# Performance work log

Hardware: AMD Instinct MI355X
Metric: run time of the kernel (lower is better)

## Reference

```python
import jax, jax.numpy as jnp
import numpy as np

EMBED = 1024
HEADS = 16
HEAD_DIM = EMBED // HEADS


def setup_inputs() -> dict:
    key = jax.random.key(0)
    ks = jax.random.split(key, 8)
    N, S = 4, 2048
    inp = {
        "values": jax.random.normal(ks[0], (N, S, EMBED), jnp.float32),
        "keys": jax.random.normal(ks[1], (N, S, EMBED), jnp.float32),
        "queries": jax.random.normal(ks[2], (N, S, EMBED), jnp.float32),
        "mask": jnp.ones((N, S), jnp.int32),  # unused by the original forward
        # learned params (torch Linear: y = x @ W.T + b)
        "Wv": jax.random.normal(ks[3], (HEAD_DIM, HEAD_DIM), jnp.float32) / np.sqrt(HEAD_DIM),
        "Wk": jax.random.normal(ks[4], (HEAD_DIM, HEAD_DIM), jnp.float32) / np.sqrt(HEAD_DIM),
        "Wq": jax.random.normal(ks[5], (HEAD_DIM, HEAD_DIM), jnp.float32) / np.sqrt(HEAD_DIM),
        "Wo": jax.random.normal(ks[6], (EMBED, EMBED), jnp.float32) / np.sqrt(EMBED),
        "bo": jax.random.normal(ks[7], (EMBED,), jnp.float32) * 0.01,
    }
    return inp


def reference(values, keys, queries, mask, Wv, Wk, Wq, Wo, bo):
    N, S, _ = queries.shape
    # reshape to (N, len, heads, head_dim)
    v = values.reshape(N, S, HEADS, HEAD_DIM)
    k = keys.reshape(N, S, HEADS, HEAD_DIM)
    q = queries.reshape(N, S, HEADS, HEAD_DIM)
    # per-head linear projections (weights shared across heads), y = x @ W.T
    v = jnp.einsum('nlhd,ed->nlhe', v, Wv)
    k = jnp.einsum('nlhd,ed->nlhe', k, Wk)
    q = jnp.einsum('nlhd,ed->nlhe', q, Wq)
    # attention scores scaled by sqrt(embed_size), faithful to original
    scores = jnp.einsum('nqhd,nkhd->nhqk', q, k) / jnp.sqrt(jnp.float32(EMBED))
    attn = jax.nn.softmax(scores, axis=3)
    out = jnp.einsum('nhql,nlhd->nqhd', attn, v).reshape(N, S, EMBED)
    return out @ Wo.T + bo
```

## Files before the change

### kernel.cpp

```cpp
#include <hip/hip_runtime.h>


using f32x4  = __attribute__((ext_vector_type(4))) float;
using f32x16 = __attribute__((ext_vector_type(16))) float;
using bf16x8 = __attribute__((ext_vector_type(8))) __bf16;
using u32x4  = __attribute__((ext_vector_type(4))) unsigned int;
using u16x8  = __attribute__((ext_vector_type(8))) unsigned short;
typedef unsigned short u16;
typedef unsigned int   u32;
typedef unsigned long long u64;

#define SEQ 2048
#define EMB 1024
#define NHEADS 16
#define HDIM 64
#define NBATCH 4
#define NH 64

__device__ __forceinline__ u16 f2bf(float f) {
  u32 u = __builtin_bit_cast(u32, f);
  return (u16)((u + 0x7fffu + ((u >> 16) & 1u)) >> 16);
}

__device__ __forceinline__ u32 cvtpk_bf16(float a, float b) {
  u32 d;
  asm("v_cvt_pk_bf16_f32 %0, %1, %2" : "=v"(d) : "v"(a), "v"(b));
  return d;
}

__device__ __forceinline__ f32x4 mfma16(bf16x8 a, bf16x8 b, f32x4 c) {
  return __builtin_amdgcn_mfma_f32_16x16x32_bf16(a, b, c, 0, 0, 0);
}

__device__ __forceinline__ f32x16 mfma32(bf16x8 a, bf16x8 b, f32x16 c) {
  return __builtin_amdgcn_mfma_f32_32x32x16_bf16(a, b, c, 0, 0, 0);
}

__device__ __forceinline__ bf16x8 cvt8(f32x4 a, f32x4 b) {
  u32x4 r;
  r[0] = cvtpk_bf16(a[0], a[1]);
  r[1] = cvtpk_bf16(a[2], a[3]);
  r[2] = cvtpk_bf16(b[0], b[1]);
  r[3] = cvtpk_bf16(b[2], b[3]);
  return __builtin_bit_cast(bf16x8, r);
}

__device__ __forceinline__ float fexp2(float x) {
  float r;
  asm("v_exp_f32 %0, %1" : "=v"(r) : "v"(x));
  return r;
}

__device__ __forceinline__ void swap_words(u32 a, u32 b, int hi, u32& wlo, u32& whi) {
#if __has_builtin(__builtin_amdgcn_permlane32_swap)
  (void)hi;
  auto rr = __builtin_amdgcn_permlane32_swap((int)a, (int)b, false, false);
  wlo = (u32)rr[0];
  whi = (u32)rr[1];
#else
  u32 pa = (u32)__shfl_xor((int)a, 32);
  u32 pb = (u32)__shfl_xor((int)b, 32);
  wlo = hi ? pb : a;
  whi = hi ? b : pa;
#endif
}

__global__ __launch_bounds__(256) void proj_kernel(
    const float* __restrict__ Xq, const float* __restrict__ Xk, const float* __restrict__ Xv,
    const float* __restrict__ Wq, const float* __restrict__ Wk, const float* __restrict__ Wv,
    u16* __restrict__ Qp, u16* __restrict__ Kp, u16* __restrict__ Vp,
    const float* __restrict__ Wo, u16* __restrict__ Wob)
{
  int which = blockIdx.y;
  if (which == 3) {
    int i = (blockIdx.x * 256 + threadIdx.x) * 2;
    float a = Wo[i], b = Wo[i + 1];
    *(u32*)(Wob + i) = cvtpk_bf16(a, b);
    return;
  }
  const float* X = which == 0 ? Xq : (which == 1 ? Xk : Xv);
  const float* W = which == 0 ? Wq : (which == 1 ? Wk : Wv);
  u16* Out = which == 0 ? Qp : (which == 1 ? Kp : Vp);
  float wscale = which == 0 ? 0.045084220027780106f : 1.0f;

  __shared__ u16 Osm[64 * 72];

  int t = threadIdx.x;
  int w = t >> 6, l = t & 63, l15 = l & 15, grp = l >> 4;
  int g0 = blockIdx.x * 64;

  bf16x8 wf[4][2];
#pragma unroll
  for (int nt = 0; nt < 4; nt++) {
    int c = nt * 16 + l15;
#pragma unroll
    for (int dc = 0; dc < 2; dc++) {
      const float* p = W + c * 64 + dc * 32 + grp * 8;
      f32x4 a = *(const f32x4*)p;
      f32x4 b = *(const f32x4*)(p + 4);
      a *= wscale; b *= wscale;
      wf[nt][dc] = cvt8(a, b);
    }
  }
  int grow = g0 + w * 16 + l15;
  const float* xr = X + (long)grow * 64;
  bf16x8 af[2];
#pragma unroll
  for (int dc = 0; dc < 2; dc++) {
    f32x4 a = *(const f32x4*)(xr + dc * 32 + grp * 8);
    f32x4 b = *(const f32x4*)(xr + dc * 32 + grp * 8 + 4);
    af[dc] = cvt8(a, b);
  }
  f32x4 acc[4] = {};
#pragma unroll
  for (int dc = 0; dc < 2; dc++)
#pragma unroll
    for (int nt = 0; nt < 4; nt++)
      acc[nt] = mfma16(af[dc], wf[nt][dc], acc[nt]);

#pragma unroll
  for (int r = 0; r < 4; r++)
#pragma unroll
    for (int nt = 0; nt < 4; nt++)
      Osm[(w * 16 + grp * 4 + r) * 72 + nt * 16 + l15] = f2bf(acc[nt][r]);

  int rl = t >> 2, qtr = t & 3;
  const char* srcp = (const char*)Osm + rl * 144 + qtr * 32;
  u32x4 v0 = *(const u32x4*)srcp;
  u32x4 v1 = *(const u32x4*)(srcp + 16);
  int g = g0 + rl;
  int n = g >> 15, s = (g >> 4) & 2047, h = g & 15;
  char* dstp = (char*)(Out + (((long)(n * NHEADS + h) * SEQ + s) << 6)) + qtr * 32;
  *(u32x4*)dstp = v0;
  *(u32x4*)(dstp + 16) = v1;
}

__global__ __launch_bounds__(256) void transpose_v(
    const u16* __restrict__ Vp, u16* __restrict__ Vt)
{
  int st = blockIdx.x;
  int nh = blockIdx.y;
  __shared__ u16 Vs[64 * 65];
  int t = threadIdx.x;
  const u16* src = Vp + ((long)nh * SEQ + st * 64) * 64;
#pragma unroll
  for (int p = 0; p < 2; p++) {
    int row = p * 32 + (t >> 3);
    int c0 = (t & 7) * 8;
    u32x4 u = *(const u32x4*)(src + row * 64 + c0);
    u16x8 v = __builtin_bit_cast(u16x8, u);
#pragma unroll
    for (int j = 0; j < 8; j++) Vs[(c0 + j) * 65 + row] = v[j];
  }
  __syncthreads();
  int e = t >> 2, k0 = (t & 3) * 16;
  u16x8 lo, hi;
#pragma unroll
  for (int j = 0; j < 8; j++) { lo[j] = Vs[e * 65 + k0 + j]; hi[j] = Vs[e * 65 + k0 + 8 + j]; }
  u16* dst = Vt + ((long)nh * 64 + e) * SEQ + st * 64 + k0;
  *(u32x4*)dst = __builtin_bit_cast(u32x4, lo);
  *(u32x4*)(dst + 8) = __builtin_bit_cast(u32x4, hi);
}


#define LDV(off) __builtin_bit_cast(bf16x8, *(const u32x4*)(smem + (off)))

#define ATTN_STEP(CUROFF, DOSTAGE, DOPREF) do {                            \
    if (DOSTAGE) {                                                         \
      *(u32x4*)(smem + sphys0 + ((CUROFF) ^ 16384)) = kreg[0];             \
      *(u32x4*)(smem + sphys1 + ((CUROFF) ^ 16384)) = kreg[1];             \
      *(u32x4*)(smem + sphys0 + 8192 + ((CUROFF) ^ 16384)) = vreg[0];      \
      *(u32x4*)(smem + sphys1 + 8192 + ((CUROFF) ^ 16384)) = vreg[1];      \
      if (DOPREF) {                                                        \
        kreg[0] = *(const u32x4*)kp0; kp0 += 8192;                         \
        kreg[1] = *(const u32x4*)kp1; kp1 += 8192;                         \
        vreg[0] = *(const u32x4*)vp0; vp0 += 128;                          \
        vreg[1] = *(const u32x4*)vp1; vp1 += 128;                          \
      }                                                                    \
    }                                                                      \
    f32x16 zz = {};                                                        \
    f32x16 s0, s1;                                                         \
    __builtin_amdgcn_s_setprio(1);                                         \
    {                                                                      \
      bf16x8 kf0 = LDV(koff[0] + (CUROFF));                                \
      bf16x8 kf1 = LDV(koff[1] + (CUROFF));                                \
      s0 = mfma32(kf0, qf[0], zz);                                         \
      s1 = mfma32(kf1, qf[0], zz);                                         \
    }                                                                      \
    _Pragma("unroll")                                                      \
    for (int dc = 1; dc < 4; dc++) {                                       \
      bf16x8 kf0 = LDV(koff[dc * 2 + 0] + (CUROFF));                       \
      bf16x8 kf1 = LDV(koff[dc * 2 + 1] + (CUROFF));                       \
      s0 = mfma32(kf0, qf[dc], s0);                                        \
      s1 = mfma32(kf1, qf[dc], s1);                                        \
    }                                                                      \
    __builtin_amdgcn_s_setprio(0);                                         \
                                    \
    _Pragma("unroll")                                                      \
    for (int r = 0; r < 16; r++) s0[r] = fexp2(s0[r]);                     \
    _Pragma("unroll")                                                      \
    for (int r = 0; r < 16; r++) s1[r] = fexp2(s1[r]);                     \
    { f32x16 ss = s0 + s1;                                                 \
      f32x4 q4 = { ss[0]+ss[4], ss[1]+ss[5], ss[2]+ss[6], ss[3]+ss[7] };   \
      f32x4 q5 = { ss[8]+ss[12], ss[9]+ss[13], ss[10]+ss[14], ss[11]+ss[15] }; \
      f32x4 q6 = q4 + q5;                                                  \
      lrun += (q6[0] + q6[1]) + (q6[2] + q6[3]); }                         \
              \
    bf16x8 pB[4];                                                          \
    { u32 xw[8], wq[16];                                                   \
      _Pragma("unroll")                                                    \
      for (int i = 0; i < 8; i++) xw[i] = cvtpk_bf16(s0[2*i], s0[2*i+1]);  \
      swap_words(xw[0], xw[2], hi, wq[0], wq[2]);                          \
      swap_words(xw[1], xw[3], hi, wq[1], wq[3]);                          \
      swap_words(xw[4], xw[6], hi, wq[4], wq[6]);                          \
      swap_words(xw[5], xw[7], hi, wq[5], wq[7]);                          \
      _Pragma("unroll")                                                    \
      for (int i = 0; i < 8; i++) xw[i] = cvtpk_bf16(s1[2*i], s1[2*i+1]);  \
      swap_words(xw[0], xw[2], hi, wq[8], wq[10]);                         \
      swap_words(xw[1], xw[3], hi, wq[9], wq[11]);                         \
      swap_words(xw[4], xw[6], hi, wq[12], wq[14]);                        \
      swap_words(xw[5], xw[7], hi, wq[13], wq[15]);                        \
      _Pragma("unroll")                                                    \
      for (int kb = 0; kb < 4; kb++) {                                     \
        u32x4 v4 = { wq[kb*4+0], wq[kb*4+1], wq[kb*4+2], wq[kb*4+3] };     \
        pB[kb] = __builtin_bit_cast(bf16x8, v4); } }                       \
                                                 \
    __builtin_amdgcn_s_setprio(1);                                         \
    _Pragma("unroll")                                                      \
    for (int kb = 0; kb < 4; kb++) {                                       \
      bf16x8 vf0 = LDV(koff[kb * 2 + 0] + 8192 + (CUROFF));                \
      bf16x8 vf1 = LDV(koff[kb * 2 + 1] + 8192 + (CUROFF));                \
      o0 = mfma32(vf0, pB[kb], o0);                                        \
      o1 = mfma32(vf1, pB[kb], o1);                                        \
    }                                                                      \
    __builtin_amdgcn_s_setprio(0);                                         \
    __syncthreads();                                                       \
  } while (0)

__global__ __launch_bounds__(256, 3) void attn_kernel(
    const u16* __restrict__ Qp, const u16* __restrict__ Kp, const u16* __restrict__ Vt,
    u16* __restrict__ AO)
{
  int nh = blockIdx.x;
  int qb = blockIdx.y;
  int n = nh >> 4, h = nh & 15;

  __shared__ __align__(16) char smem[32768];

  int t = threadIdx.x, w = t >> 6, l = t & 63;
  int l31 = l & 31, hi = l >> 5;

  long qrow = (long)nh * SEQ + qb * 128 + w * 32 + l31;
  const char* qbase = (const char*)Qp + qrow * 128;
  bf16x8 qf[4];
#pragma unroll
  for (int dc = 0; dc < 4; dc++)
    qf[dc] = __builtin_bit_cast(bf16x8, *(const u32x4*)(qbase + dc * 32 + hi * 16));

  f32x16 o0 = {}, o1 = {};
  float lrun = 0.f;

  int koff[8];
#pragma unroll
  for (int dc = 0; dc < 4; dc++)
#pragma unroll
    for (int half = 0; half < 2; half++) {
      int row = half * 32 + l31;
      int cc = dc * 2 + hi;
      koff[dc * 2 + half] = row * 128 + ((cc ^ (row & 7)) << 4);
    }

  int sr0 = t >> 3, sc = t & 7, sr1 = sr0 + 32;
  int sphys0 = sr0 * 128 + ((sc ^ (sr0 & 7)) << 4);
  int sphys1 = sr1 * 128 + ((sc ^ (sr1 & 7)) << 4);

  const char* Kg = (const char*)(Kp + (long)nh * SEQ * 64);
  const char* Vg = (const char*)(Vt + (long)nh * 64 * SEQ);
  const char* kp0 = Kg + sr0 * 128 + sc * 16;
  const char* kp1 = Kg + sr1 * 128 + sc * 16;
  const char* vp0 = Vg + (long)sr0 * 4096 + sc * 16;
  const char* vp1 = Vg + (long)sr1 * 4096 + sc * 16;

  u32x4 kreg[2], vreg[2];
  kreg[0] = *(const u32x4*)kp0;
  kreg[1] = *(const u32x4*)kp1;
  vreg[0] = *(const u32x4*)vp0;
  vreg[1] = *(const u32x4*)vp1;
  *(u32x4*)(smem + sphys0) = kreg[0];
  *(u32x4*)(smem + sphys1) = kreg[1];
  *(u32x4*)(smem + 8192 + sphys0) = vreg[0];
  *(u32x4*)(smem + 8192 + sphys1) = vreg[1];
  kreg[0] = *(const u32x4*)(kp0 + 8192); kp0 += 16384;
  kreg[1] = *(const u32x4*)(kp1 + 8192); kp1 += 16384;
  vreg[0] = *(const u32x4*)(vp0 + 128);  vp0 += 256;
  vreg[1] = *(const u32x4*)(vp1 + 128);  vp1 += 256;
  __syncthreads();

  for (int kt2 = 0; kt2 < 16; kt2++) {
    ATTN_STEP(0, true, (kt2 < 15));
    ATTN_STEP(16384, (kt2 < 15), (kt2 < 15));
  }

  lrun += __shfl_xor(lrun, 32);
  float inv = 1.0f / lrun;
  int qlocal = w * 32 + l31;
  char* OsmB = smem;
#pragma unroll
  for (int i = 0; i < 8; i++) {
    int e0 = ((2 * i) & 3) + 8 * ((2 * i) >> 2) + 4 * hi;
    *(u32*)(OsmB + qlocal * 144 + 2 * e0) = cvtpk_bf16(o0[2*i] * inv, o0[2*i+1] * inv);
    *(u32*)(OsmB + qlocal * 144 + 2 * (e0 + 32)) = cvtpk_bf16(o1[2*i] * inv, o1[2*i+1] * inv);
  }
  __syncthreads();
  int qr = t >> 1, half = t & 1;
  const char* src = OsmB + qr * 144 + half * 64;
  long qg = (long)qb * 128 + qr;
  char* dst = (char*)(AO + ((long)n * SEQ + qg) * EMB + h * 64 + half * 32);
#pragma unroll
  for (int j = 0; j < 4; j++)
    *(u32x4*)(dst + j * 16) = *(const u32x4*)(src + j * 16);
}

__global__ __launch_bounds__(256) void gemm_out(
    const u16* __restrict__ A, const u16* __restrict__ B,
    const float* __restrict__ bias, float* __restrict__ C)
{
  int bm0 = blockIdx.x;
  int bm = (bm0 & 7) * 8 + (bm0 >> 3);
  int bn = blockIdx.y;
  __shared__ __align__(16) char gsm[65536];
  int t = threadIdx.x, w = t >> 6, l = t & 63;
  int l31 = l & 31, hi = l >> 5;
  int wm = w >> 1, wn = w & 1;
  f32x16 acc[2][2] = {};
  const char* Ab = (const char*)(A + (long)bm * 128 * 1024);
  const char* Bb = (const char*)(B + (long)bn * 128 * 1024);

  int cphys[4];
  long cgoff[4];
#pragma unroll
  for (int p = 0; p < 4; p++) {
    int i = t + p * 256;
    int row = i >> 3, c = i & 7;
    cphys[p] = row * 128 + ((c ^ (row & 7)) << 4);
    cgoff[p] = (long)row * 2048 + c * 16;
  }

  int aoff[2][4], boff[2][4];
#pragma unroll
  for (int ti = 0; ti < 2; ti++)
#pragma unroll
    for (int kk = 0; kk < 4; kk++) {
      int rowa = wm * 64 + ti * 32 + l31;
      int rowb = wn * 64 + ti * 32 + l31;
      int c = kk * 2 + hi;
      aoff[ti][kk] = rowa * 128 + ((c ^ (rowa & 7)) << 4);
      boff[ti][kk] = 16384 + rowb * 128 + ((c ^ (rowb & 7)) << 4);
    }

  u32x4 areg[4], breg[4];
#pragma unroll
  for (int p = 0; p < 4; p++) {
    areg[p] = *(const u32x4*)(Ab + cgoff[p]);
    breg[p] = *(const u32x4*)(Bb + cgoff[p]);
  }
#pragma unroll
  for (int p = 0; p < 4; p++) {
    *(u32x4*)(gsm + cphys[p]) = areg[p];
    *(u32x4*)(gsm + 16384 + cphys[p]) = breg[p];
  }
#pragma unroll
  for (int p = 0; p < 4; p++) {
    areg[p] = *(const u32x4*)(Ab + cgoff[p] + 128);
    breg[p] = *(const u32x4*)(Bb + cgoff[p] + 128);
  }
  __syncthreads();

  for (int kt = 0; kt < 16; kt++) {
    const char* cur = gsm + ((kt & 1) << 15);
    char* nxt = gsm + (((kt + 1) & 1) << 15);

    if (kt + 1 < 16) {
#pragma unroll
      for (int p = 0; p < 4; p++) {
        *(u32x4*)(nxt + cphys[p]) = areg[p];
        *(u32x4*)(nxt + 16384 + cphys[p]) = breg[p];
      }
      if (kt + 2 < 16) {
#pragma unroll
        for (int p = 0; p < 4; p++) {
          areg[p] = *(const u32x4*)(Ab + cgoff[p] + (kt + 2) * 128);
          breg[p] = *(const u32x4*)(Bb + cgoff[p] + (kt + 2) * 128);
        }
      }
    }

    __builtin_amdgcn_s_setprio(1);
#pragma unroll
    for (int kk = 0; kk < 4; kk++) {
      bf16x8 af0 = __builtin_bit_cast(bf16x8, *(const u32x4*)(cur + aoff[0][kk]));
      bf16x8 af1 = __builtin_bit_cast(bf16x8, *(const u32x4*)(cur + aoff[1][kk]));
      bf16x8 bf0 = __builtin_bit_cast(bf16x8, *(const u32x4*)(cur + boff[0][kk]));
      bf16x8 bf1 = __builtin_bit_cast(bf16x8, *(const u32x4*)(cur + boff[1][kk]));
      acc[0][0] = mfma32(af0, bf0, acc[0][0]);
      acc[0][1] = mfma32(af0, bf1, acc[0][1]);
      acc[1][0] = mfma32(af1, bf0, acc[1][0]);
      acc[1][1] = mfma32(af1, bf1, acc[1][1]);
    }
    __builtin_amdgcn_s_setprio(0);

    __syncthreads();
  }

  float bv[2];
#pragma unroll
  for (int tj = 0; tj < 2; tj++) bv[tj] = bias[bn * 128 + wn * 64 + tj * 32 + l31];
#pragma unroll
  for (int ti = 0; ti < 2; ti++)
#pragma unroll
    for (int tj = 0; tj < 2; tj++) {
#pragma unroll
      for (int r = 0; r < 16; r++) {
        long row = (long)bm * 128 + wm * 64 + ti * 32 + ((r & 3) + 8 * (r >> 2) + 4 * hi);
        C[row * 1024 + bn * 128 + wn * 64 + tj * 32 + l31] = acc[ti][tj][r] + bv[tj];
      }
    }
}

extern "C" void kernel_launch(void* const* d_in, const int* in_sizes, int n_in,
                              void* d_out, int out_size, void* d_ws, size_t ws_size,
                              hipStream_t stream)
{
  const float* Vx = (const float*)d_in[0];
  const float* Kx = (const float*)d_in[1];
  const float* Qx = (const float*)d_in[2];
  const float* Wv = (const float*)d_in[4];
  const float* Wk = (const float*)d_in[5];
  const float* Wq = (const float*)d_in[6];
  const float* Wo = (const float*)d_in[7];
  const float* bo = (const float*)d_in[8];
  float* out = (float*)d_out;
  char* ws = (char*)d_ws;

  u16* Qp  = (u16*)(ws);
  u16* Kp  = (u16*)(ws + (1L << 24));
  u16* Vt  = (u16*)(ws + (2L << 24));
  u16* Vp  = (u16*)(ws + (3L << 24));
  u16* AO  = Vp;
  u16* Wob = (u16*)(ws + (4L << 24));

  proj_kernel<<<dim3(2048, 4), 256, 0, stream>>>(Qx, Kx, Vx, Wq, Wk, Wv, Qp, Kp, Vp, Wo, Wob);
  transpose_v<<<dim3(32, 64), 256, 0, stream>>>(Vp, Vt);
  attn_kernel<<<dim3(64, 16), 256, 0, stream>>>(Qp, Kp, Vt, AO);
  gemm_out<<<dim3(64, 8), 256, 0, stream>>>(AO, Wob, bo, out);
}
```

Measured before the change: 171.9 us.

## Stage two K/V tiles per barrier to halve attention loop syncs

The attention loop now stages two 64-key K/V tiles at once into a 64KB double-buffered LDS region and processes both before a single __syncthreads, instead of one tile per barrier. This halves the number of block-wide barriers and deepens the global prefetch to two tiles in registers. In exchange it doubles shared memory per block and raises register pressure, with launch bounds lowered from 3 to 2 blocks per CU, which reduces occupancy.

```diff
diff --git a/kernel.cpp b/kernel.cpp
--- a/kernel.cpp
+++ b/kernel.cpp
@@ -165,32 +165,20 @@
 
 #define LDV(off) __builtin_bit_cast(bf16x8, *(const u32x4*)(smem + (off)))
 
-#define ATTN_STEP(CUROFF, DOSTAGE, DOPREF) do {                            \
-    if (DOSTAGE) {                                                         \
-      *(u32x4*)(smem + sphys0 + ((CUROFF) ^ 16384)) = kreg[0];             \
-      *(u32x4*)(smem + sphys1 + ((CUROFF) ^ 16384)) = kreg[1];             \
-      *(u32x4*)(smem + sphys0 + 8192 + ((CUROFF) ^ 16384)) = vreg[0];      \
-      *(u32x4*)(smem + sphys1 + 8192 + ((CUROFF) ^ 16384)) = vreg[1];      \
-      if (DOPREF) {                                                        \
-        kreg[0] = *(const u32x4*)kp0; kp0 += 8192;                         \
-        kreg[1] = *(const u32x4*)kp1; kp1 += 8192;                         \
-        vreg[0] = *(const u32x4*)vp0; vp0 += 128;                          \
-        vreg[1] = *(const u32x4*)vp1; vp1 += 128;                          \
-      }                                                                    \
-    }                                                                      \
+#define ATTN_COMP(KOFF) do {                                               \
     f32x16 zz = {};                                                        \
     f32x16 s0, s1;                                                         \
     __builtin_amdgcn_s_setprio(1);                                         \
     {                                                                      \
-      bf16x8 kf0 = LDV(koff[0] + (CUROFF));                                \
-      bf16x8 kf1 = LDV(koff[1] + (CUROFF));                                \
+      bf16x8 kf0 = LDV(koff[0] + (KOFF));                                  \
+      bf16x8 kf1 = LDV(koff[1] + (KOFF));                                  \
       s0 = mfma32(kf0, qf[0], zz);                                         \
       s1 = mfma32(kf1, qf[0], zz);                                         \
     }                                                                      \
     _Pragma("unroll")                                                      \
     for (int dc = 1; dc < 4; dc++) {                                       \
-      bf16x8 kf0 = LDV(koff[dc * 2 + 0] + (CUROFF));                       \
-      bf16x8 kf1 = LDV(koff[dc * 2 + 1] + (CUROFF));                       \
+      bf16x8 kf0 = LDV(koff[dc * 2 + 0] + (KOFF));                         \
+      bf16x8 kf1 = LDV(koff[dc * 2 + 1] + (KOFF));                         \
       s0 = mfma32(kf0, qf[dc], s0);                                        \
       s1 = mfma32(kf1, qf[dc], s1);                                        \
     }                                                                      \
@@ -228,16 +216,41 @@
     __builtin_amdgcn_s_setprio(1);                                         \
     _Pragma("unroll")                                                      \
     for (int kb = 0; kb < 4; kb++) {                                       \
-      bf16x8 vf0 = LDV(koff[kb * 2 + 0] + 8192 + (CUROFF));                \
-      bf16x8 vf1 = LDV(koff[kb * 2 + 1] + 8192 + (CUROFF));                \
+      bf16x8 vf0 = LDV(koff[kb * 2 + 0] + 8192 + (KOFF));                  \
+      bf16x8 vf1 = LDV(koff[kb * 2 + 1] + 8192 + (KOFF));                  \
       o0 = mfma32(vf0, pB[kb], o0);                                        \
       o1 = mfma32(vf1, pB[kb], o1);                                        \
     }                                                                      \
     __builtin_amdgcn_s_setprio(0);                                         \
-    __syncthreads();                                                       \
   } while (0)
 
-__global__ __launch_bounds__(256, 3) void attn_kernel(
+#define ATTN_STAGE2(DST, DOPREF) do {                                     \
+    *(u32x4*)(smem + sphys0 + (DST)) = kA[0];                             \
+    *(u32x4*)(smem + sphys1 + (DST)) = kA[1];                             \
+    *(u32x4*)(smem + sphys0 + 8192 + (DST)) = vA[0];                      \
+    *(u32x4*)(smem + sphys1 + 8192 + (DST)) = vA[1];                      \
+    *(u32x4*)(smem + sphys0 + 16384 + (DST)) = kB[0];                     \
+    *(u32x4*)(smem + sphys1 + 16384 + (DST)) = kB[1];                     \
+    *(u32x4*)(smem + sphys0 + 24576 + (DST)) = vB[0];                     \
+    *(u32x4*)(smem + sphys1 + 24576 + (DST)) = vB[1];                     \
+    if (DOPREF) {                                                         \
+      kA[0] = *(const u32x4*)kp0;          kA[1] = *(const u32x4*)kp1;    \
+      kB[0] = *(const u32x4*)(kp0 + 8192); kB[1] = *(const u32x4*)(kp1 + 8192); \
+      kp0 += 16384; kp1 += 16384;                                         \
+      vA[0] = *(const u32x4*)vp0;          vA[1] = *(const u32x4*)vp1;    \
+      vB[0] = *(const u32x4*)(vp0 + 128);  vB[1] = *(const u32x4*)(vp1 + 128);  \
+      vp0 += 256; vp1 += 256;                                             \
+    }                                                                     \
+  } while (0)
+
+#define ATTN_PAIR(CUR, DOSTAGE, DOPREF) do {                              \
+    if (DOSTAGE) ATTN_STAGE2((CUR) ^ 32768, DOPREF);                      \
+    ATTN_COMP(CUR);                                                       \
+    ATTN_COMP((CUR) + 16384);                                             \
+    __syncthreads();                                                      \
+  } while (0)
+
+__global__ __launch_bounds__(256, 2) void attn_kernel(
     const u16* __restrict__ Qp, const u16* __restrict__ Kp, const u16* __restrict__ Vt,
     u16* __restrict__ AO)
 {
@@ -245,7 +258,7 @@
   int qb = blockIdx.y;
   int n = nh >> 4, h = nh & 15;
 
-  __shared__ __align__(16) char smem[32768];
+  __shared__ __align__(16) char smem[65536];
 
   int t = threadIdx.x, w = t >> 6, l = t & 63;
   int l31 = l & 31, hi = l >> 5;
@@ -281,24 +294,19 @@
   const char* vp0 = Vg + (long)sr0 * 4096 + sc * 16;
   const char* vp1 = Vg + (long)sr1 * 4096 + sc * 16;
 
-  u32x4 kreg[2], vreg[2];
-  kreg[0] = *(const u32x4*)kp0;
-  kreg[1] = *(const u32x4*)kp1;
-  vreg[0] = *(const u32x4*)vp0;
-  vreg[1] = *(const u32x4*)vp1;
-  *(u32x4*)(smem + sphys0) = kreg[0];
-  *(u32x4*)(smem + sphys1) = kreg[1];
-  *(u32x4*)(smem + 8192 + sphys0) = vreg[0];
-  *(u32x4*)(smem + 8192 + sphys1) = vreg[1];
-  kreg[0] = *(const u32x4*)(kp0 + 8192); kp0 += 16384;
-  kreg[1] = *(const u32x4*)(kp1 + 8192); kp1 += 16384;
-  vreg[0] = *(const u32x4*)(vp0 + 128);  vp0 += 256;
-  vreg[1] = *(const u32x4*)(vp1 + 128);  vp1 += 256;
+  u32x4 kA[2], kB[2], vA[2], vB[2];
+  kA[0] = *(const u32x4*)kp0;          kA[1] = *(const u32x4*)kp1;
+  kB[0] = *(const u32x4*)(kp0 + 8192); kB[1] = *(const u32x4*)(kp1 + 8192);
+  kp0 += 16384; kp1 += 16384;
+  vA[0] = *(const u32x4*)vp0;          vA[1] = *(const u32x4*)vp1;
+  vB[0] = *(const u32x4*)(vp0 + 128);  vB[1] = *(const u32x4*)(vp1 + 128);
+  vp0 += 256; vp1 += 256;
+  ATTN_STAGE2(0, true);
   __syncthreads();
 
-  for (int kt2 = 0; kt2 < 16; kt2++) {
-    ATTN_STEP(0, true, (kt2 < 15));
-    ATTN_STEP(16384, (kt2 < 15), (kt2 < 15));
+  for (int i2 = 0; i2 < 8; i2++) {
+    ATTN_PAIR(0, true, (i2 < 7));
+    ATTN_PAIR(32768, (i2 < 7), (i2 < 7));
   }
 
   lrun += __shfl_xor(lrun, 32);
```

Result: no change. 174.8 us (+1.7%).
